# Kernel tuning notes

Measured on AMD Instinct MI355X. Metric: run time of the kernel, lower is better.

The kernel has to match this reference:

```python
import jax, jax.numpy as jnp
import numpy as np

FFT_SIZE = 2046
MSE_WEIGHT = 0.7
DELAY_WEIGHT = 0.3
ENERGY_EPS = 1e-8
RANGE_EPS = 1e-8
TEMP_SCALE = 10.0


def setup_inputs() -> dict:
    key = jax.random.key(0)
    k1, k2 = jax.random.split(key)
    shape = (32, 64, 4, 1024)  # [batch, bs_ant, ue_ant, subcarriers]
    predicted_csi = jax.random.normal(k1, shape, dtype=jnp.float32)
    target_csi = jax.random.normal(k2, shape, dtype=jnp.float32)
    return {"predicted_csi": predicted_csi, "target_csi": target_csi}


def _compute_pdp(csi):
    # Real input is treated as complex with zero imaginary part (as in torch module).
    n = csi.shape[-1]
    if n < FFT_SIZE:
        pad = [(0, 0)] * (csi.ndim - 1) + [(0, FFT_SIZE - n)]
        csi = jnp.pad(csi, pad)
    else:
        csi = csi[..., :FFT_SIZE]
    td = jnp.fft.ifft(csi.astype(jnp.complex64), axis=-1)  # [..., FFT_SIZE]
    return jnp.abs(td) ** 2


def _normalize_pdp(pdp):
    # Per-sample (last-axis) energy normalization; skip if energy ~ 0.
    energy = jnp.sum(pdp, axis=-1, keepdims=True)
    return jnp.where(energy < ENERGY_EPS, pdp, pdp / energy)


def _soft_delay(pdp):
    # Adaptive-temperature soft-argmax delay per sample.
    f = pdp.shape[-1]
    idx = jnp.arange(f, dtype=jnp.float32)
    rng = jnp.clip(jnp.max(pdp, -1, keepdims=True) - jnp.min(pdp, -1, keepdims=True), RANGE_EPS)
    weights = jax.nn.softmax(pdp * (TEMP_SCALE / rng), axis=-1)
    return jnp.sum(idx * weights, axis=-1)


def reference(predicted_csi, target_csi):
    pdp_pred = _normalize_pdp(_compute_pdp(predicted_csi))  # [B, BS, UE, FFT_SIZE]
    pdp_tgt = _normalize_pdp(_compute_pdp(target_csi))
    # MSE per sample is mean over FFT_SIZE; averaging over samples/antenna pairs == global mean.
    mse_loss = jnp.mean((pdp_pred - pdp_tgt) ** 2)
    delay_diff = jnp.abs(_soft_delay(pdp_pred) - _soft_delay(pdp_tgt)) / FFT_SIZE
    delay_loss = jnp.mean(delay_diff)
    return MSE_WEIGHT * mse_loss + DELAY_WEIGHT * delay_loss
```

## Files before the change

kernel.cpp:

```cpp
#include <hip/hip_runtime.h>
#include <math.h>

#define IN_N   1024
#define NROWS  8192
#define NTOT   16384
#define FFT_N  2046

typedef unsigned short u16;
typedef __attribute__((ext_vector_type(8))) __bf16 bf16x8;
typedef __attribute__((ext_vector_type(4))) float  f32x4;

__device__ __forceinline__ u16 f2bf(float f) {
    unsigned u = __builtin_bit_cast(unsigned, f);
    unsigned r = (u + 0x7fffu + ((u >> 16) & 1u)) >> 16;
    return (u16)r;
}
__device__ __forceinline__ float bf2f(u16 h) {
    unsigned u = ((unsigned)h) << 16;
    return __builtin_bit_cast(float, u);
}

__device__ __forceinline__ void gload_lds16(const void* g, void* l) {
    __builtin_amdgcn_global_load_lds(
        (__attribute__((address_space(1))) void*)g,
        (__attribute__((address_space(3))) void*)l, 16, 0, 0);
}

__global__ void twiddle_kernel(u16* __restrict__ Wc, u16* __restrict__ Ws) {
    int k = blockIdx.x;
    int n0 = threadIdx.x * 4;
    const float c = 6.28318530717958647692f / 2046.0f;
    ushort4 oc, os;
    #pragma unroll
    for (int i = 0; i < 4; ++i) {
        int n = n0 + i;
        int m = (k * n) % FFT_N;
        float a = (float)m * c;
        float sv, cv;
        sincosf(a, &sv, &cv);
        ((u16*)&oc)[i] = f2bf(cv);
        ((u16*)&os)[i] = f2bf(sv);
    }
    size_t o = (size_t)k * IN_N + n0;
    *(ushort4*)(Wc + o) = oc;
    *(ushort4*)(Ws + o) = os;
}

__global__ __launch_bounds__(256) void convert_kernel(
    const float* __restrict__ pred, const float* __restrict__ tgt,
    u16* __restrict__ Xh) {
    size_t gid = (size_t)blockIdx.x * 256 + threadIdx.x;
    size_t e = gid * 4;
    const size_t half = (size_t)NROWS * IN_N;
    const float* s = (e < half) ? (pred + e) : (tgt + (e - half));
    float4 v = *(const float4*)s;
    ushort4 o;
    o.x = f2bf(v.x); o.y = f2bf(v.y); o.z = f2bf(v.z); o.w = f2bf(v.w);
    *(ushort4*)(Xh + e) = o;
}

#define BM 128
#define BN 256
#define BK 32
#define NKT 32

__global__ __launch_bounds__(512, 2) void dft_pdp_mfma(
    const u16* __restrict__ Wc, const u16* __restrict__ Ws,
    const u16* __restrict__ Xh, u16* __restrict__ pdp) {

    __shared__ __align__(16) char lds[4][32768];

    const int bid  = blockIdx.x;
    const int xcd  = bid & 7;
    const int slot = bid >> 3;
    const int m0 = (slot & 7) * BM;
    const int r0 = (xcd * 8 + (slot >> 3)) * BN;

    const int t    = threadIdx.x;
    const int w    = t >> 6;
    const int lane = t & 63;
    const int wm = (w & 1) * 64;
    const int wr = (w >> 1) * 64;
    const int lr = lane & 15;
    const int rdoff = (((lane >> 4) ^ ((lane >> 1) & 3)) << 4);

    const int srow  = t >> 2;
    const int sslot = (t & 3) ^ ((t >> 3) & 3);
    const size_t aOfs  = (size_t)(m0 + srow) * 2048 + sslot * 16;
    const size_t xOfs0 = (size_t)(r0 + srow) * 2048 + sslot * 16;
    const size_t xOfs1 = (size_t)(r0 + 128 + srow) * 2048 + sslot * 16;
    const int woff = w << 10;

    f32x4 accRe[4][4], accIm[4][4];
    #pragma unroll
    for (int i = 0; i < 4; ++i)
        #pragma unroll
        for (int j = 0; j < 4; ++j)
            #pragma unroll
            for (int q = 0; q < 4; ++q) { accRe[i][j][q] = 0.f; accIm[i][j][q] = 0.f; }

    #define STAGE_A(buf, kt) do { \
        gload_lds16((const char*)Wc + aOfs + (size_t)(kt) * 64, &lds[buf][0] + woff); \
        gload_lds16((const char*)Ws + aOfs + (size_t)(kt) * 64, &lds[buf][0] + 8192 + woff); \
    } while (0)
    #define STAGE_X(buf, kt) do { \
        gload_lds16((const char*)Xh + xOfs0 + (size_t)(kt) * 64, &lds[buf][0] + 16384 + woff); \
        gload_lds16((const char*)Xh + xOfs1 + (size_t)(kt) * 64, &lds[buf][0] + 24576 + woff); \
    } while (0)

    STAGE_A(0, 0); STAGE_X(0, 0);
    STAGE_A(1, 1); STAGE_X(1, 1);
    STAGE_A(2, 2); STAGE_X(2, 2);
    asm volatile("s_waitcnt vmcnt(8)" ::: "memory");
    __builtin_amdgcn_s_barrier();

    for (int kt = 0; kt < NKT; ++kt) {
        const int  buf = kt & 3;
        const char* bA = &lds[buf][0];
        const char* bS = &lds[buf][0] + 8192;
        const char* bX = &lds[buf][0] + 16384;
        const bool st  = (kt + 3) < NKT;
        const int  sb  = (kt + 3) & 3;

        bf16x8 fb[4], fa0, fa1, fs0, fs1;
        #pragma unroll
        for (int j = 0; j < 4; ++j)
            fb[j] = *(const bf16x8*)(bX + (wr + j * 16 + lr) * 64 + rdoff);
        fa0 = *(const bf16x8*)(bA + (wm +  0 + lr) * 64 + rdoff);
        fa1 = *(const bf16x8*)(bA + (wm + 16 + lr) * 64 + rdoff);
        fs0 = *(const bf16x8*)(bS + (wm +  0 + lr) * 64 + rdoff);
        fs1 = *(const bf16x8*)(bS + (wm + 16 + lr) * 64 + rdoff);
        if (st) STAGE_A(sb, kt + 3);
        __builtin_amdgcn_s_barrier();
        asm volatile("s_waitcnt lgkmcnt(0)" ::: "memory");
        __builtin_amdgcn_sched_barrier(0);
        __builtin_amdgcn_s_setprio(1);
        #pragma unroll
        for (int j = 0; j < 4; ++j) {
            accRe[0][j] = __builtin_amdgcn_mfma_f32_16x16x32_bf16(fa0, fb[j], accRe[0][j], 0, 0, 0);
            accIm[0][j] = __builtin_amdgcn_mfma_f32_16x16x32_bf16(fs0, fb[j], accIm[0][j], 0, 0, 0);
        }
        #pragma unroll
        for (int j = 0; j < 4; ++j) {
            accRe[1][j] = __builtin_amdgcn_mfma_f32_16x16x32_bf16(fa1, fb[j], accRe[1][j], 0, 0, 0);
            accIm[1][j] = __builtin_amdgcn_mfma_f32_16x16x32_bf16(fs1, fb[j], accIm[1][j], 0, 0, 0);
        }
        __builtin_amdgcn_s_setprio(0);
        __builtin_amdgcn_s_barrier();

        bf16x8 fa2, fa3, fs2, fs3;
        fa2 = *(const bf16x8*)(bA + (wm + 32 + lr) * 64 + rdoff);
        fa3 = *(const bf16x8*)(bA + (wm + 48 + lr) * 64 + rdoff);
        fs2 = *(const bf16x8*)(bS + (wm + 32 + lr) * 64 + rdoff);
        fs3 = *(const bf16x8*)(bS + (wm + 48 + lr) * 64 + rdoff);
        if (st) STAGE_X(sb, kt + 3);
        __builtin_amdgcn_s_barrier();
        asm volatile("s_waitcnt lgkmcnt(0)" ::: "memory");
        __builtin_amdgcn_sched_barrier(0);
        __builtin_amdgcn_s_setprio(1);
        #pragma unroll
        for (int j = 0; j < 4; ++j) {
            accRe[2][j] = __builtin_amdgcn_mfma_f32_16x16x32_bf16(fa2, fb[j], accRe[2][j], 0, 0, 0);
            accIm[2][j] = __builtin_amdgcn_mfma_f32_16x16x32_bf16(fs2, fb[j], accIm[2][j], 0, 0, 0);
        }
        #pragma unroll
        for (int j = 0; j < 4; ++j) {
            accRe[3][j] = __builtin_amdgcn_mfma_f32_16x16x32_bf16(fa3, fb[j], accRe[3][j], 0, 0, 0);
            accIm[3][j] = __builtin_amdgcn_mfma_f32_16x16x32_bf16(fs3, fb[j], accIm[3][j], 0, 0, 0);
        }
        __builtin_amdgcn_s_setprio(0);
        if (kt <= 28)      asm volatile("s_waitcnt vmcnt(8)" ::: "memory");
        else if (kt == 29) asm volatile("s_waitcnt vmcnt(4)" ::: "memory");
        else if (kt == 30) asm volatile("s_waitcnt vmcnt(0)" ::: "memory");
        __builtin_amdgcn_s_barrier();
    }
    #undef STAGE_A
    #undef STAGE_X

    const float inv = 1.0f / ((float)FFT_N * (float)FFT_N);
    #pragma unroll
    for (int i = 0; i < 4; ++i)
        #pragma unroll
        for (int j = 0; j < 4; ++j) {
            int m = m0 + wm + i * 16 + (lane >> 4) * 4;
            int r = r0 + wr + j * 16 + (lane & 15);
            ushort4 o;
            #pragma unroll
            for (int q = 0; q < 4; ++q) {
                float re = accRe[i][j][q], im = accIm[i][j][q];
                ((u16*)&o)[q] = f2bf((re * re + im * im) * inv);
            }
            *(ushort4*)(pdp + (size_t)r * IN_N + m) = o;
        }
}

__device__ __forceinline__ float breduce(float v, float* red, int t, int op) {
    __syncthreads();
    red[t] = v;
    __syncthreads();
    for (int s = 128; s > 0; s >>= 1) {
        if (t < s) {
            float x = red[t], y = red[t + s];
            red[t] = (op == 0) ? (x + y) : (op == 1) ? fmaxf(x, y) : fminf(x, y);
        }
        __syncthreads();
    }
    return red[0];
}

__global__ __launch_bounds__(256) void row_stats_kernel(
    const u16* __restrict__ pdp,
    float* __restrict__ mse_rows, float* __restrict__ dd_rows) {

    __shared__ float red[256];
    const int r = blockIdx.x;
    const int t = threadIdx.x;
    const u16* pp = pdp + (size_t)r * IN_N;
    const u16* pt = pdp + (size_t)(NROWS + r) * IN_N;
    ushort4 up = *(const ushort4*)(pp + t * 4);
    ushort4 ut = *(const ushort4*)(pt + t * 4);
    float a[4] = {bf2f(up.x), bf2f(up.y), bf2f(up.z), bf2f(up.w)};
    float b[4] = {bf2f(ut.x), bf2f(ut.y), bf2f(ut.z), bf2f(ut.w)};

    float wsp = 0.f, wst = 0.f;
    float mxp = -1e30f, mnp = 1e30f, mxt = -1e30f, mnt = 1e30f;
    #pragma unroll
    for (int i = 0; i < 4; ++i) {
        int k = t * 4 + i;
        float wgt = (k == 0 || k == 1023) ? 1.f : 2.f;
        wsp += wgt * a[i];        wst += wgt * b[i];
        mxp = fmaxf(mxp, a[i]);   mnp = fminf(mnp, a[i]);
        mxt = fmaxf(mxt, b[i]);   mnt = fminf(mnt, b[i]);
    }
    float Ep  = breduce(wsp, red, t, 0);
    float Et  = breduce(wst, red, t, 0);
    float Mp  = breduce(mxp, red, t, 1);
    float mp_ = breduce(mnp, red, t, 2);
    float Mt  = breduce(mxt, red, t, 1);
    float mt_ = breduce(mnt, red, t, 2);

    float scp = (Ep < 1e-8f) ? 1.f : 1.f / Ep;
    float sct = (Et < 1e-8f) ? 1.f : 1.f / Et;
    float rngp = fmaxf(scp * (Mp - mp_), 1e-8f);
    float rngt = fmaxf(sct * (Mt - mt_), 1e-8f);
    float cfp = 10.f * scp / rngp;
    float cft = 10.f * sct / rngt;
    float smp = cfp * Mp;
    float smt = cft * Mt;

    float zp = 0.f, zt = 0.f, ms = 0.f;
    #pragma unroll
    for (int i = 0; i < 4; ++i) {
        int k = t * 4 + i;
        float wgt = (k == 0 || k == 1023) ? 1.f : 2.f;
        zp += wgt * expf(cfp * a[i] - smp);
        zt += wgt * expf(cft * b[i] - smt);
        float d = a[i] * scp - b[i] * sct;
        ms += wgt * d * d;
    }
    float Zp  = breduce(zp, red, t, 0);
    float Zt  = breduce(zt, red, t, 0);
    float MSE = breduce(ms, red, t, 0);

    if (t == 0) {
        float w0p = expf(cfp * a[0] - smp) / Zp;
        float w0t = expf(cft * b[0] - smt) / Zt;
        mse_rows[r] = MSE;
        dd_rows[r]  = 0.5f * fabsf(w0p - w0t);
    }
}

__global__ __launch_bounds__(256) void final_kernel(
    const float* __restrict__ mse_rows, const float* __restrict__ dd_rows,
    float* __restrict__ out) {
    __shared__ float r1[256];
    __shared__ float r2[256];
    int t = threadIdx.x;
    float s1 = 0.f, s2 = 0.f;
    for (int r = t; r < NROWS; r += 256) { s1 += mse_rows[r]; s2 += dd_rows[r]; }
    r1[t] = s1; r2[t] = s2;
    __syncthreads();
    for (int s = 128; s > 0; s >>= 1) {
        if (t < s) { r1[t] += r1[t + s]; r2[t] += r2[t + s]; }
        __syncthreads();
    }
    if (t == 0) {
        float mse = r1[0] / ((float)NROWS * (float)FFT_N);
        float dl  = r2[0] / (float)NROWS;
        out[0] = 0.7f * mse + 0.3f * dl;
    }
}

extern "C" void kernel_launch(void* const* d_in, const int* in_sizes, int n_in,
                              void* d_out, int out_size, void* d_ws, size_t ws_size,
                              hipStream_t stream) {
    const float* pred = (const float*)d_in[0];
    const float* tgt  = (const float*)d_in[1];
    float* out = (float*)d_out;

    char* ws = (char*)d_ws;
    u16* Xh   = (u16*)ws;
    u16* Wch  = (u16*)(ws + (size_t)32 * 1024 * 1024);
    u16* Wsh  = (u16*)(ws + (size_t)34 * 1024 * 1024);
    u16* pdp  = (u16*)(ws + (size_t)40 * 1024 * 1024);
    float* mse_rows = (float*)(ws + (size_t)72 * 1024 * 1024);
    float* dd_rows  = mse_rows + NROWS;

    twiddle_kernel<<<1024, 256, 0, stream>>>(Wch, Wsh);
    convert_kernel<<<NTOT * IN_N / 4 / 256, 256, 0, stream>>>(pred, tgt, Xh);

    dft_pdp_mfma<<<512, 512, 0, stream>>>(Wch, Wsh, Xh, pdp);

    row_stats_kernel<<<NROWS, 256, 0, stream>>>(pdp, mse_rows, dd_rows);
    final_kernel<<<1, 256, 0, stream>>>(mse_rows, dd_rows, out);
}
```

Baseline: 138.7 us.

## Prefetch next k-tile LDS fragments across barriers and halve barriers per iteration

Restructures the MFMA main loop into a software pipeline. The A/S fragments and X fragments for the next k-tile are read from LDS during the current tile's MFMA phases, and partial lgkmcnt waits replace full drains. The loop now uses two workgroup barriers per k-step instead of four, and the vmcnt thresholds are retuned to match the new order of issued global-to-LDS loads. The aim is to hide LDS read latency and barrier stalls behind MFMA work, at the cost of more live registers and fragile hand-counted wait counts that must keep the buffer reuse race-free.

Result: no change. 137.0 us (-1.2%).

```diff
diff --git a/kernel.cpp b/kernel.cpp
--- a/kernel.cpp
+++ b/kernel.cpp
@@ -64,6 +64,8 @@
 #define BK 32
 #define NKT 32
 
+#define FENCE() asm volatile("" ::: "memory")
+
 __global__ __launch_bounds__(512, 2) void dft_pdp_mfma(
     const u16* __restrict__ Wc, const u16* __restrict__ Ws,
     const u16* __restrict__ Xh, u16* __restrict__ pdp) {
@@ -107,75 +109,95 @@
         gload_lds16((const char*)Xh + xOfs0 + (size_t)(kt) * 64, &lds[buf][0] + 16384 + woff); \
         gload_lds16((const char*)Xh + xOfs1 + (size_t)(kt) * 64, &lds[buf][0] + 24576 + woff); \
     } while (0)
+    #define LDA(buf, off) (*(const bf16x8*)(&lds[buf][0] + (wm + (off) + lr) * 64 + rdoff))
+    #define LDSN(buf, off) (*(const bf16x8*)(&lds[buf][0] + 8192 + (wm + (off) + lr) * 64 + rdoff))
+    #define LDX(buf, j)   (*(const bf16x8*)(&lds[buf][0] + 16384 + (wr + (j) * 16 + lr) * 64 + rdoff))
 
     STAGE_A(0, 0); STAGE_X(0, 0);
     STAGE_A(1, 1); STAGE_X(1, 1);
     STAGE_A(2, 2); STAGE_X(2, 2);
     asm volatile("s_waitcnt vmcnt(8)" ::: "memory");
     __builtin_amdgcn_s_barrier();
+    FENCE();
+
+    bf16x8 fb0, fb1, fb2, fb3, fa0, fa1, fa2, fa3, fs0, fs1, fs2, fs3;
+    fb0 = LDX(0, 0); fb1 = LDX(0, 1); fb2 = LDX(0, 2); fb3 = LDX(0, 3);
+    fa0 = LDA(0, 0); fa1 = LDA(0, 16); fs0 = LDSN(0, 0); fs1 = LDSN(0, 16);
 
     for (int kt = 0; kt < NKT; ++kt) {
-        const int  buf = kt & 3;
-        const char* bA = &lds[buf][0];
-        const char* bS = &lds[buf][0] + 8192;
-        const char* bX = &lds[buf][0] + 16384;
-        const bool st  = (kt + 3) < NKT;
-        const int  sb  = (kt + 3) & 3;
-
-        bf16x8 fb[4], fa0, fa1, fs0, fs1;
-        #pragma unroll
-        for (int j = 0; j < 4; ++j)
-            fb[j] = *(const bf16x8*)(bX + (wr + j * 16 + lr) * 64 + rdoff);
-        fa0 = *(const bf16x8*)(bA + (wm +  0 + lr) * 64 + rdoff);
-        fa1 = *(const bf16x8*)(bA + (wm + 16 + lr) * 64 + rdoff);
-        fs0 = *(const bf16x8*)(bS + (wm +  0 + lr) * 64 + rdoff);
-        fs1 = *(const bf16x8*)(bS + (wm + 16 + lr) * 64 + rdoff);
+        const int bcur  = kt & 3;
+        const int bnext = (kt + 1) & 3;
+        const int sb    = (kt + 3) & 3;
+        const bool st   = (kt + 3) < NKT;
+        const bool more = (kt + 1) < NKT;
+
+        fa2 = LDA(bcur, 32); fa3 = LDA(bcur, 48);
+        fs2 = LDSN(bcur, 32); fs3 = LDSN(bcur, 48);
         if (st) STAGE_A(sb, kt + 3);
-        __builtin_amdgcn_s_barrier();
-        asm volatile("s_waitcnt lgkmcnt(0)" ::: "memory");
+        asm volatile("s_waitcnt lgkmcnt(4)" ::: "memory");
         __builtin_amdgcn_sched_barrier(0);
         __builtin_amdgcn_s_setprio(1);
-        #pragma unroll
-        for (int j = 0; j < 4; ++j) {
-            accRe[0][j] = __builtin_amdgcn_mfma_f32_16x16x32_bf16(fa0, fb[j], accRe[0][j], 0, 0, 0);
-            accIm[0][j] = __builtin_amdgcn_mfma_f32_16x16x32_bf16(fs0, fb[j], accIm[0][j], 0, 0, 0);
+        accRe[0][0] = __builtin_amdgcn_mfma_f32_16x16x32_bf16(fa0, fb0, accRe[0][0], 0, 0, 0);
+        accIm[0][0] = __builtin_amdgcn_mfma_f32_16x16x32_bf16(fs0, fb0, accIm[0][0], 0, 0, 0);
+        accRe[0][1] = __builtin_amdgcn_mfma_f32_16x16x32_bf16(fa0, fb1, accRe[0][1], 0, 0, 0);
+        accIm[0][1] = __builtin_amdgcn_mfma_f32_16x16x32_bf16(fs0, fb1, accIm[0][1], 0, 0, 0);
+        accRe[0][2] = __builtin_amdgcn_mfma_f32_16x16x32_bf16(fa0, fb2, accRe[0][2], 0, 0, 0);
+        accIm[0][2] = __builtin_amdgcn_mfma_f32_16x16x32_bf16(fs0, fb2, accIm[0][2], 0, 0, 0);
+        accRe[0][3] = __builtin_amdgcn_mfma_f32_16x16x32_bf16(fa0, fb3, accRe[0][3], 0, 0, 0);
+        accIm[0][3] = __builtin_amdgcn_mfma_f32_16x16x32_bf16(fs0, fb3, accIm[0][3], 0, 0, 0);
+        accRe[1][0] = __builtin_amdgcn_mfma_f32_16x16x32_bf16(fa1, fb0, accRe[1][0], 0, 0, 0);
+        accIm[1][0] = __builtin_amdgcn_mfma_f32_16x16x32_bf16(fs1, fb0, accIm[1][0], 0, 0, 0);
+        accRe[1][1] = __builtin_amdgcn_mfma_f32_16x16x32_bf16(fa1, fb1, accRe[1][1], 0, 0, 0);
+        accIm[1][1] = __builtin_amdgcn_mfma_f32_16x16x32_bf16(fs1, fb1, accIm[1][1], 0, 0, 0);
+        accRe[1][2] = __builtin_amdgcn_mfma_f32_16x16x32_bf16(fa1, fb2, accRe[1][2], 0, 0, 0);
+        accIm[1][2] = __builtin_amdgcn_mfma_f32_16x16x32_bf16(fs1, fb2, accIm[1][2], 0, 0, 0);
+        accRe[1][3] = __builtin_amdgcn_mfma_f32_16x16x32_bf16(fa1, fb3, accRe[1][3], 0, 0, 0);
+        accIm[1][3] = __builtin_amdgcn_mfma_f32_16x16x32_bf16(fs1, fb3, accIm[1][3], 0, 0, 0);
+        __builtin_amdgcn_s_setprio(0);
+
+        if (kt <= NKT - 4)      asm volatile("s_waitcnt vmcnt(6)" ::: "memory");
+        else if (kt == NKT - 3) asm volatile("s_waitcnt vmcnt(4)" ::: "memory");
+        else                    asm volatile("s_waitcnt vmcnt(0)" ::: "memory");
+        __builtin_amdgcn_s_barrier();
+        FENCE();
+        if (more) {
+            fa0 = LDA(bnext, 0); fa1 = LDA(bnext, 16);
+            fs0 = LDSN(bnext, 0); fs1 = LDSN(bnext, 16);
         }
-        #pragma unroll
-        for (int j = 0; j < 4; ++j) {
-            accRe[1][j] = __builtin_amdgcn_mfma_f32_16x16x32_bf16(fa1, fb[j], accRe[1][j], 0, 0, 0);
-            accIm[1][j] = __builtin_amdgcn_mfma_f32_16x16x32_bf16(fs1, fb[j], accIm[1][j], 0, 0, 0);
-        }
-        __builtin_amdgcn_s_setprio(0);
-        __builtin_amdgcn_s_barrier();
-
-        bf16x8 fa2, fa3, fs2, fs3;
-        fa2 = *(const bf16x8*)(bA + (wm + 32 + lr) * 64 + rdoff);
-        fa3 = *(const bf16x8*)(bA + (wm + 48 + lr) * 64 + rdoff);
-        fs2 = *(const bf16x8*)(bS + (wm + 32 + lr) * 64 + rdoff);
-        fs3 = *(const bf16x8*)(bS + (wm + 48 + lr) * 64 + rdoff);
         if (st) STAGE_X(sb, kt + 3);
-        __builtin_amdgcn_s_barrier();
-        asm volatile("s_waitcnt lgkmcnt(0)" ::: "memory");
+        if (more) asm volatile("s_waitcnt lgkmcnt(4)" ::: "memory");
+        else      asm volatile("s_waitcnt lgkmcnt(0)" ::: "memory");
         __builtin_amdgcn_sched_barrier(0);
         __builtin_amdgcn_s_setprio(1);
-        #pragma unroll
-        for (int j = 0; j < 4; ++j) {
-            accRe[2][j] = __builtin_amdgcn_mfma_f32_16x16x32_bf16(fa2, fb[j], accRe[2][j], 0, 0, 0);
-            accIm[2][j] = __builtin_amdgcn_mfma_f32_16x16x32_bf16(fs2, fb[j], accIm[2][j], 0, 0, 0);
+        accRe[2][0] = __builtin_amdgcn_mfma_f32_16x16x32_bf16(fa2, fb0, accRe[2][0], 0, 0, 0);
+        accIm[2][0] = __builtin_amdgcn_mfma_f32_16x16x32_bf16(fs2, fb0, accIm[2][0], 0, 0, 0);
+        accRe[2][1] = __builtin_amdgcn_mfma_f32_16x16x32_bf16(fa2, fb1, accRe[2][1], 0, 0, 0);
+        accIm[2][1] = __builtin_amdgcn_mfma_f32_16x16x32_bf16(fs2, fb1, accIm[2][1], 0, 0, 0);
+        accRe[2][2] = __builtin_amdgcn_mfma_f32_16x16x32_bf16(fa2, fb2, accRe[2][2], 0, 0, 0);
+        accIm[2][2] = __builtin_amdgcn_mfma_f32_16x16x32_bf16(fs2, fb2, accIm[2][2], 0, 0, 0);
+        accRe[2][3] = __builtin_amdgcn_mfma_f32_16x16x32_bf16(fa2, fb3, accRe[2][3], 0, 0, 0);
+        accIm[2][3] = __builtin_amdgcn_mfma_f32_16x16x32_bf16(fs2, fb3, accIm[2][3], 0, 0, 0);
+        accRe[3][0] = __builtin_amdgcn_mfma_f32_16x16x32_bf16(fa3, fb0, accRe[3][0], 0, 0, 0);
+        accIm[3][0] = __builtin_amdgcn_mfma_f32_16x16x32_bf16(fs3, fb0, accIm[3][0], 0, 0, 0);
+        accRe[3][1] = __builtin_amdgcn_mfma_f32_16x16x32_bf16(fa3, fb1, accRe[3][1], 0, 0, 0);
+        accIm[3][1] = __builtin_amdgcn_mfma_f32_16x16x32_bf16(fs3, fb1, accIm[3][1], 0, 0, 0);
+        accRe[3][2] = __builtin_amdgcn_mfma_f32_16x16x32_bf16(fa3, fb2, accRe[3][2], 0, 0, 0);
+        accIm[3][2] = __builtin_amdgcn_mfma_f32_16x16x32_bf16(fs3, fb2, accIm[3][2], 0, 0, 0);
+        accRe[3][3] = __builtin_amdgcn_mfma_f32_16x16x32_bf16(fa3, fb3, accRe[3][3], 0, 0, 0);
+        accIm[3][3] = __builtin_amdgcn_mfma_f32_16x16x32_bf16(fs3, fb3, accIm[3][3], 0, 0, 0);
+        __builtin_amdgcn_s_setprio(0);
+        if (more) {
+            fb0 = LDX(bnext, 0); fb1 = LDX(bnext, 1);
+            fb2 = LDX(bnext, 2); fb3 = LDX(bnext, 3);
         }
-        #pragma unroll
-        for (int j = 0; j < 4; ++j) {
-            accRe[3][j] = __builtin_amdgcn_mfma_f32_16x16x32_bf16(fa3, fb[j], accRe[3][j], 0, 0, 0);
-            accIm[3][j] = __builtin_amdgcn_mfma_f32_16x16x32_bf16(fs3, fb[j], accIm[3][j], 0, 0, 0);
-        }
-        __builtin_amdgcn_s_setprio(0);
-        if (kt <= 28)      asm volatile("s_waitcnt vmcnt(8)" ::: "memory");
-        else if (kt == 29) asm volatile("s_waitcnt vmcnt(4)" ::: "memory");
-        else if (kt == 30) asm volatile("s_waitcnt vmcnt(0)" ::: "memory");
         __builtin_amdgcn_s_barrier();
+        FENCE();
     }
     #undef STAGE_A
     #undef STAGE_X
+    #undef LDA
+    #undef LDSN
+    #undef LDX
 
     const float inv = 1.0f / ((float)FFT_N * (float)FFT_N);
     #pragma unroll
```
